# Kernel tuning notes

Measured on AMD Instinct MI355X. Metric: run time of the kernel, lower is better.

## Reference

```python
import jax, jax.numpy as jnp
import numpy as np

B, S, H = 2, 2048, 2048
NH, KVH, HD = 16, 4, 128
R = 16
LORA_SCALE = 32.0 / 16.0  # lora_alpha / lora_r
ATTN_SCALE = HD ** -0.5
NEG = -1e9


def setup_inputs() -> dict:
    key = jax.random.key(0)
    ks = jax.random.split(key, 16)
    q_dim, kv_dim = NH * HD, KVH * HD
    # RoPE tables
    inv_freq = 1.0 / (10000.0 ** (jnp.arange(0, HD, 2, dtype=jnp.float32) / HD))
    ang = jnp.arange(S, dtype=jnp.float32)[:, None] * inv_freq[None, :]  # [S, HD/2]
    emb = jnp.concatenate([ang, ang], axis=-1)  # [S, HD]
    cos = jnp.broadcast_to(jnp.cos(emb)[None], (B, S, HD))
    sin = jnp.broadcast_to(jnp.sin(emb)[None], (B, S, HD))
    # additive causal mask [B,1,S,S]
    causal = jnp.triu(jnp.full((S, S), NEG, dtype=jnp.float32), k=1)
    attention_mask = jnp.broadcast_to(causal[None, None], (B, 1, S, S))
    return {
        'hidden_states': jax.random.normal(ks[0], (B, S, H), jnp.float32),
        'cos': cos,
        'sin': sin,
        'attention_mask': attention_mask,
        'q_w': jax.random.normal(ks[1], (q_dim, H), jnp.float32) * 0.02,
        'k_w': jax.random.normal(ks[2], (kv_dim, H), jnp.float32) * 0.02,
        'v_w': jax.random.normal(ks[3], (kv_dim, H), jnp.float32) * 0.02,
        'q_b': jax.random.normal(ks[4], (q_dim,), jnp.float32) * 0.02,
        'k_b': jax.random.normal(ks[5], (kv_dim,), jnp.float32) * 0.02,
        'v_b': jax.random.normal(ks[6], (kv_dim,), jnp.float32) * 0.02,
        'q_A': jax.random.normal(ks[7], (H, R), jnp.float32) * (1.0 / np.sqrt(H)),
        'q_B': jax.random.normal(ks[8], (R, q_dim), jnp.float32) * 0.02,
        'k_A': jax.random.normal(ks[9], (H, R), jnp.float32) * (1.0 / np.sqrt(H)),
        'k_B': jax.random.normal(ks[10], (R, kv_dim), jnp.float32) * 0.02,
        'v_A': jax.random.normal(ks[11], (H, R), jnp.float32) * (1.0 / np.sqrt(H)),
        'v_B': jax.random.normal(ks[12], (R, kv_dim), jnp.float32) * 0.02,
        'o_w': jax.random.normal(ks[13], (H, H), jnp.float32) * 0.02,
    }


def _rotate_half(x):
    x1, x2 = x[..., : HD // 2], x[..., HD // 2:]
    return jnp.concatenate([-x2, x1], axis=-1)


def reference(hidden_states, cos, sin, attention_mask,
              q_w, k_w, v_w, q_b, k_b, v_b,
              q_A, q_B, k_A, k_B, v_A, v_B, o_w):
    x = hidden_states  # dropout p=0 (eval)
    # fused base + LoRA projections
    q = x @ q_w.T + q_b + LORA_SCALE * ((x @ q_A) @ q_B)  # [B,S,NH*HD]
    k = x @ k_w.T + k_b + LORA_SCALE * ((x @ k_A) @ k_B)  # [B,S,KVH*HD]
    v = x @ v_w.T + v_b + LORA_SCALE * ((x @ v_A) @ v_B)
    q = q.reshape(B, S, NH, HD).transpose(0, 2, 1, 3)   # [B,NH,S,HD]
    k = k.reshape(B, S, KVH, HD).transpose(0, 2, 1, 3)  # [B,KVH,S,HD]
    v = v.reshape(B, S, KVH, HD).transpose(0, 2, 1, 3)
    # RoPE
    c = cos[:, None]  # [B,1,S,HD]
    s = sin[:, None]
    q = q * c + _rotate_half(q) * s
    k = k * c + _rotate_half(k) * s
    # GQA: repeat kv heads
    n_rep = NH // KVH
    k = jnp.repeat(k, n_rep, axis=1)  # [B,NH,S,HD]
    v = jnp.repeat(v, n_rep, axis=1)
    scores = jnp.einsum('bhqd,bhkd->bhqk', q, k) * ATTN_SCALE
    scores = scores + attention_mask
    attn = jax.nn.softmax(scores.astype(jnp.float32), axis=-1).astype(q.dtype)
    out = jnp.einsum('bhqk,bhkd->bhqd', attn, v)
    out = out.transpose(0, 2, 1, 3).reshape(B, S, NH * HD)  # [B,S,H]
    return out @ o_w.T
```

## Files before the change

kernel.cpp:

```cpp
#include <hip/hip_runtime.h>

constexpr int cB   = 2;
constexpr int cS   = 2048;
constexpr int cH   = 2048;
constexpr int cNH  = 16;
constexpr int cKVH = 4;
constexpr int cHD  = 128;
constexpr int cQD  = 2048;
constexpr int cKVD = 512;
constexpr int cNQKV = 3072;
constexpr int cNTOK = 4096;
#define ATTN_SCALE 0.08838834764831845f

typedef __bf16 bf16;
typedef __attribute__((ext_vector_type(8))) __bf16 bf16x8;
typedef __attribute__((ext_vector_type(4))) __bf16 bf16x4;
typedef __attribute__((ext_vector_type(4))) float  f32x4;

__device__ __forceinline__ void async_load16(const bf16* g, bf16* l) {
    __builtin_amdgcn_global_load_lds(
        (const __attribute__((address_space(1))) void*)g,
        (__attribute__((address_space(3))) void*)l, 16, 0, 0);
}

__global__ void conv_f32_bf16(const float* __restrict__ in, bf16* __restrict__ out) {
    int i = (blockIdx.x * 256 + threadIdx.x) * 4;
    f32x4 v = *(const f32x4*)(in + i);
    bf16x4 o;
    o[0] = (bf16)v[0]; o[1] = (bf16)v[1]; o[2] = (bf16)v[2]; o[3] = (bf16)v[3];
    *(bf16x4*)(out + i) = o;
}

__global__ void prep_w(const float* __restrict__ qw, const float* __restrict__ kw, const float* __restrict__ vw,
                       const float* __restrict__ qA, const float* __restrict__ qB,
                       const float* __restrict__ kA, const float* __restrict__ kB,
                       const float* __restrict__ vA, const float* __restrict__ vB,
                       bf16* __restrict__ Wc) {
    const int idx = blockIdx.x * 256 + threadIdx.x;
    const int n = idx >> 11, k = idx & 2047;
    const float* W; const float* Am; const float* Bm; int nn, nd;
    if (n < cQD)             { W = qw; Am = qA; Bm = qB; nn = n;          nd = cQD; }
    else if (n < cQD + cKVD) { W = kw; Am = kA; Bm = kB; nn = n - cQD;    nd = cKVD; }
    else                     { W = vw; Am = vA; Bm = vB; nn = n - cQD - cKVD; nd = cKVD; }
    float acc = 0.f;
    #pragma unroll
    for (int r = 0; r < 16; ++r) acc += Am[k * 16 + r] * Bm[r * nd + nn];
    Wc[(size_t)n * cH + k] = (bf16)(W[(size_t)nn * cH + k] + 2.0f * acc);
}

__global__ void prep_bias(const float* __restrict__ qb, const float* __restrict__ kb,
                          const float* __restrict__ vb, float* __restrict__ biasc) {
    int n = blockIdx.x * 256 + threadIdx.x;
    if (n >= cNQKV) return;
    biasc[n] = (n < cQD) ? qb[n] : (n < cQD + cKVD ? kb[n - cQD] : vb[n - cQD - cKVD]);
}

__global__ __launch_bounds__(256) void gemm_qkv(const bf16* __restrict__ A, const bf16* __restrict__ Bw,
                                                const float* __restrict__ bias,
                                                const float* __restrict__ cosb, const float* __restrict__ sinb,
                                                bf16* __restrict__ Qr, bf16* __restrict__ Kr,
                                                bf16* __restrict__ Vt) {
    __shared__ bf16 Al[128 * 32];
    __shared__ bf16 Bl[128 * 32];
    const int tid = threadIdx.x;
    const int wave = tid >> 6, lane = tid & 63;
    const int quad = lane >> 4, l16 = lane & 15;
    const int wr = wave >> 1, wc = wave & 1;
    const long bm = (long)blockIdx.y * 128, bn = (long)blockIdx.x * 128;
    const int K = cH;

    f32x4 acc[4][4];
    #pragma unroll
    for (int i = 0; i < 4; ++i)
        #pragma unroll
        for (int c = 0; c < 4; ++c) acc[i][c] = f32x4{0.f, 0.f, 0.f, 0.f};

    const int r0 = lane >> 2;
    const int kc = (lane & 3) * 8;

    for (int k0 = 0; k0 < K; k0 += 32) {
        __syncthreads();
        #pragma unroll
        for (int j = 0; j < 2; ++j) {
            const int rb = (wave * 2 + j) * 16;
            const int row = rb + r0;
            async_load16(A  + (size_t)(bm + row) * K + k0 + kc, &Al[rb * 32 + r0 * 32 + kc]);
            async_load16(Bw + (size_t)(bn + row) * K + k0 + kc, &Bl[rb * 32 + r0 * 32 + kc]);
        }
        __syncthreads();
        bf16x8 af[4], bfr[4];
        #pragma unroll
        for (int i = 0; i < 4; ++i) af[i]  = *(const bf16x8*)&Al[(wr * 64 + i * 16 + l16) * 32 + quad * 8];
        #pragma unroll
        for (int c = 0; c < 4; ++c) {
            const int nrow = wc * 32 + (c & 1) * 16 + (c >> 1) * 64 + l16;
            bfr[c] = *(const bf16x8*)&Bl[nrow * 32 + quad * 8];
        }
        #pragma unroll
        for (int i = 0; i < 4; ++i)
            #pragma unroll
            for (int c = 0; c < 4; ++c)
                acc[i][c] = __builtin_amdgcn_mfma_f32_16x16x32_bf16(af[i], bfr[c], acc[i][c], 0, 0, 0);
    }

    #pragma unroll
    for (int c = 0; c < 4; ++c) {
        const int nloc = wc * 32 + (c & 1) * 16 + (c >> 1) * 64 + l16;
        const float bv = bias[bn + nloc];
        #pragma unroll
        for (int i = 0; i < 4; ++i)
            #pragma unroll
            for (int r = 0; r < 4; ++r) acc[i][c][r] += bv;
    }

    const int head = (int)(bn >> 7);
    if (head < cNH + cKVH) {
        const bool isQ = head < cNH;
        #pragma unroll
        for (int cl = 0; cl < 2; ++cl) {
            const int d = wc * 32 + cl * 16 + l16;
            #pragma unroll
            for (int i = 0; i < 4; ++i)
                #pragma unroll
                for (int r = 0; r < 4; ++r) {
                    const long t = bm + wr * 64 + i * 16 + quad * 4 + r;
                    const float cv = cosb[t * cHD + d];
                    const float sv = sinb[t * cHD + d];
                    const float v1 = acc[i][cl][r], v2 = acc[i][cl + 2][r];
                    float o1 = v1 * cv - v2 * sv;
                    float o2 = v2 * cv + v1 * sv;
                    if (isQ) { o1 *= ATTN_SCALE; o2 *= ATTN_SCALE; }
                    const int b = (int)(t >> 11), s = (int)(t & 2047);
                    bf16* dst = isQ
                        ? Qr + ((size_t)(b * cNH + head) * cS + s) * cHD
                        : Kr + ((size_t)(b * cKVH + (head - cNH)) * cS + s) * cHD;
                    dst[d]      = (bf16)o1;
                    dst[d + 64] = (bf16)o2;
                }
        }
    } else {
        const int kv = head - cNH - cKVH;
        const int b = (int)(bm >> 11);
        const int sbase = (int)(bm & 2047);
        #pragma unroll
        for (int c = 0; c < 4; ++c) {
            const int d = wc * 32 + (c & 1) * 16 + (c >> 1) * 64 + l16;
            #pragma unroll
            for (int i = 0; i < 4; ++i) {
                const int s0 = sbase + wr * 64 + i * 16 + quad * 4;
                bf16x4 o4;
                #pragma unroll
                for (int r = 0; r < 4; ++r) o4[r] = (bf16)acc[i][c][r];
                *(bf16x4*)&Vt[((size_t)((b * cKVH + kv) * cHD) + d) * cS + s0] = o4;
            }
        }
    }
}

__global__ __launch_bounds__(256) void gemm_bt_f32(const bf16* __restrict__ A, const bf16* __restrict__ Bw,
                                                   float* __restrict__ Cp, int M, int N, int K) {
    __shared__ bf16 Al[128 * 32];
    __shared__ bf16 Bl[128 * 32];
    const int tid = threadIdx.x;
    const int wave = tid >> 6, lane = tid & 63;
    const int quad = lane >> 4, l16 = lane & 15;
    const int wr = wave >> 1, wc = wave & 1;
    const long bm = (long)blockIdx.y * 128, bn = (long)blockIdx.x * 128;

    f32x4 acc[4][4];
    #pragma unroll
    for (int i = 0; i < 4; ++i)
        #pragma unroll
        for (int c = 0; c < 4; ++c) acc[i][c] = f32x4{0.f, 0.f, 0.f, 0.f};

    const int r0 = lane >> 2;
    const int kc = (lane & 3) * 8;

    for (int k0 = 0; k0 < K; k0 += 32) {
        __syncthreads();
        #pragma unroll
        for (int j = 0; j < 2; ++j) {
            const int rb = (wave * 2 + j) * 16;
            const int row = rb + r0;
            async_load16(A  + (size_t)(bm + row) * K + k0 + kc, &Al[rb * 32 + r0 * 32 + kc]);
            async_load16(Bw + (size_t)(bn + row) * K + k0 + kc, &Bl[rb * 32 + r0 * 32 + kc]);
        }
        __syncthreads();
        bf16x8 af[4], bfr[4];
        #pragma unroll
        for (int i = 0; i < 4; ++i) af[i]  = *(const bf16x8*)&Al[(wr * 64 + i * 16 + l16) * 32 + quad * 8];
        #pragma unroll
        for (int c = 0; c < 4; ++c) bfr[c] = *(const bf16x8*)&Bl[(wc * 64 + c * 16 + l16) * 32 + quad * 8];
        #pragma unroll
        for (int i = 0; i < 4; ++i)
            #pragma unroll
            for (int c = 0; c < 4; ++c)
                acc[i][c] = __builtin_amdgcn_mfma_f32_16x16x32_bf16(af[i], bfr[c], acc[i][c], 0, 0, 0);
    }

    #pragma unroll
    for (int i = 0; i < 4; ++i)
        #pragma unroll
        for (int c = 0; c < 4; ++c) {
            const long m0 = bm + wr * 64 + i * 16 + quad * 4;
            const long n  = bn + wc * 64 + c * 16 + l16;
            #pragma unroll
            for (int r = 0; r < 4; ++r)
                Cp[(m0 + r) * N + n] = acc[i][c][r];
        }
}

__global__ __launch_bounds__(256, 2) void flash4(const bf16* __restrict__ Q, const bf16* __restrict__ K,
                                                 const bf16* __restrict__ Vt, bf16* __restrict__ Ob) {
    __shared__ bf16 kb[8192];
    __shared__ bf16 vb[8192];
    __shared__ bf16 pb[4096];
    const int tid = threadIdx.x;
    const int wave = tid >> 6, lane = tid & 63;
    const int quad = lane >> 4, l16 = lane & 15;
    const int pi = blockIdx.x;
    const int h = blockIdx.y, b = blockIdx.z;

    const bf16* Qh = Q  + (size_t)(b * cNH + h) * cS * cHD;
    const bf16* Kg = K  + (size_t)(b * cKVH + (h >> 2)) * cS * cHD;
    const bf16* Vg = Vt + (size_t)(b * cKVH + (h >> 2)) * cHD * cS;

    int kgo[4], vgo[4], slo[4];
    #pragma unroll
    for (int i2 = 0; i2 < 4; ++i2) {
        const int si = i2 * 256 + tid;
        const int krow = si >> 4, kcsw = si & 15;
        const int kc = (kcsw & 8) | ((kcsw & 7) ^ (krow & 7));
        kgo[i2] = krow * cHD + kc * 8;
        const int vrow = si >> 3, vcsw = si & 7;
        const int vc = vcsw ^ (vrow & 7);
        vgo[i2] = vrow * cS + vc * 8;
        slo[i2] = si * 8;
    }

    #pragma unroll
    for (int t2 = 0; t2 < 2; ++t2) {
        const int qt = t2 == 0 ? (31 - pi) : pi;

        const bf16* Qg = Qh + (size_t)qt * 64 * cHD;
        bf16x8 qf[4];
        #pragma unroll
        for (int ks = 0; ks < 4; ++ks)
            qf[ks] = *(const bf16x8*)(Qg + (size_t)(wave * 16 + l16) * cHD + ks * 32 + quad * 8);

        f32x4 oac[8];
        #pragma unroll
        for (int dt = 0; dt < 8; ++dt) oac[dt] = f32x4{0.f, 0.f, 0.f, 0.f};
        float m_ = -3.0e38f, l_ = 0.f;

        const int nkt = qt + 1;
        for (int kt = 0; kt < nkt; ++kt) {
            __syncthreads();
            const bf16* Kt  = Kg + (size_t)kt * 64 * cHD;
            const bf16* Vtt = Vg + kt * 64;
            #pragma unroll
            for (int i2 = 0; i2 < 4; ++i2) async_load16(Kt + kgo[i2], kb + slo[i2]);
            #pragma unroll
            for (int i2 = 0; i2 < 4; ++i2) async_load16(Vtt + vgo[i2], vb + slo[i2]);
            __syncthreads();

            f32x4 st[4];
            #pragma unroll
            for (int mt = 0; mt < 4; ++mt) {
                bf16x8 kf[4];
                #pragma unroll
                for (int ks = 0; ks < 4; ++ks) {
                    const int c = ks * 4 + quad;
                    const int csw = (c & 8) | ((c & 7) ^ (l16 & 7));
                    kf[ks] = *(const bf16x8*)&kb[(mt * 16 + l16) * 128 + csw * 8];
                }
                f32x4 a = f32x4{0.f, 0.f, 0.f, 0.f};
                #pragma unroll
                for (int ks = 0; ks < 4; ++ks)
                    a = __builtin_amdgcn_mfma_f32_16x16x32_bf16(kf[ks], qf[ks], a, 0, 0, 0);
                st[mt] = a;
            }

            const int qpos = qt * 64 + wave * 16 + l16;
            const bool dm = (kt * 64 + 63) > (qt * 64 + wave * 16);
            float tmax = -3.0e38f;
            #pragma unroll
            for (int mt = 0; mt < 4; ++mt)
                #pragma unroll
                for (int r = 0; r < 4; ++r) {
                    float v = st[mt][r];
                    if (dm) {
                        const int kpos = kt * 64 + mt * 16 + quad * 4 + r;
                        if (kpos > qpos) v = -3.0e38f;
                    }
                    st[mt][r] = v;
                    tmax = fmaxf(tmax, v);
                }
            tmax = fmaxf(tmax, __shfl_xor(tmax, 16, 64));
            tmax = fmaxf(tmax, __shfl_xor(tmax, 32, 64));
            const float mnew = fmaxf(m_, tmax);
            const float alpha = __expf(m_ - mnew);
            m_ = mnew;
            float rs = 0.f;
            #pragma unroll
            for (int mt = 0; mt < 4; ++mt)
                #pragma unroll
                for (int r = 0; r < 4; ++r) {
                    const float p = __expf(st[mt][r] - mnew);
                    st[mt][r] = p;
                    rs += p;
                }
            rs += __shfl_xor(rs, 16, 64);
            rs += __shfl_xor(rs, 32, 64);
            l_ = l_ * alpha + rs;
            #pragma unroll
            for (int dt = 0; dt < 8; ++dt)
                #pragma unroll
                for (int r = 0; r < 4; ++r) oac[dt][r] *= alpha;

            #pragma unroll
            for (int mt = 0; mt < 4; ++mt) {
                bf16x4 p4;
                #pragma unroll
                for (int r = 0; r < 4; ++r) p4[r] = (bf16)st[mt][r];
                const int csw = (mt * 2 + (quad >> 1)) ^ (l16 & 7);
                *(bf16x4*)&pb[wave * 1024 + l16 * 64 + csw * 8 + (quad & 1) * 4] = p4;
            }

            bf16x8 pf[2];
            #pragma unroll
            for (int ks = 0; ks < 2; ++ks) {
                const int c = ks * 4 + quad;
                const int csw = c ^ (l16 & 7);
                pf[ks] = *(const bf16x8*)&pb[wave * 1024 + l16 * 64 + csw * 8];
            }
            #pragma unroll
            for (int dt = 0; dt < 8; ++dt) {
                bf16x8 vf[2];
                #pragma unroll
                for (int ks = 0; ks < 2; ++ks) {
                    const int c = ks * 4 + quad;
                    const int csw = c ^ (l16 & 7);
                    vf[ks] = *(const bf16x8*)&vb[(dt * 16 + l16) * 64 + csw * 8];
                }
                #pragma unroll
                for (int ks = 0; ks < 2; ++ks)
                    oac[dt] = __builtin_amdgcn_mfma_f32_16x16x32_bf16(vf[ks], pf[ks], oac[dt], 0, 0, 0);
            }
        }

        const float inv = 1.0f / l_;
        const int token = qt * 64 + wave * 16 + l16;
        bf16* orow = Ob + (size_t)(b * cS + token) * (cNH * cHD) + h * cHD;
        #pragma unroll
        for (int dt = 0; dt < 8; ++dt) {
            bf16x4 o4;
            #pragma unroll
            for (int r = 0; r < 4; ++r) o4[r] = (bf16)(oac[dt][r] * inv);
            *(bf16x4*)&orow[dt * 16 + quad * 4] = o4;
        }
    }
}

extern "C" void kernel_launch(void* const* d_in, const int* in_sizes, int n_in,
                              void* d_out, int out_size, void* d_ws, size_t ws_size,
                              hipStream_t stream) {
    const float* x    = (const float*)d_in[0];
    const float* cosb = (const float*)d_in[1];
    const float* sinb = (const float*)d_in[2];
    const float* qw = (const float*)d_in[4];
    const float* kw = (const float*)d_in[5];
    const float* vw = (const float*)d_in[6];
    const float* qb = (const float*)d_in[7];
    const float* kb_ = (const float*)d_in[8];
    const float* vb = (const float*)d_in[9];
    const float* qA = (const float*)d_in[10];
    const float* qB = (const float*)d_in[11];
    const float* kA = (const float*)d_in[12];
    const float* kB = (const float*)d_in[13];
    const float* vA = (const float*)d_in[14];
    const float* vB = (const float*)d_in[15];
    const float* ow = (const float*)d_in[16];
    float* out = (float*)d_out;

    char* ws = (char*)d_ws;
    bf16* Xbf   = (bf16*)ws;  ws += (size_t)cNTOK * cH * 2;
    bf16* Wc    = (bf16*)ws;  ws += (size_t)cNQKV * cH * 2;
    float* biasc = (float*)ws; ws += (size_t)cNQKV * 4;
    bf16* Qr    = (bf16*)ws;  ws += (size_t)cB * cNH * cS * cHD * 2;
    bf16* Kr    = (bf16*)ws;  ws += (size_t)cB * cKVH * cS * cHD * 2;
    bf16* Vt    = (bf16*)ws;  ws += (size_t)cB * cKVH * cHD * cS * 2;
    bf16* OWbf  = (bf16*)ws;  ws += (size_t)cH * cH * 2;
    bf16* Aout  = (bf16*)ws;  ws += (size_t)cNTOK * cQD * 2;

    conv_f32_bf16<<<(cNTOK * cH) / 1024, 256, 0, stream>>>(x, Xbf);
    conv_f32_bf16<<<(cH * cH) / 1024, 256, 0, stream>>>(ow, OWbf);
    prep_w<<<(cNQKV * cH) / 256, 256, 0, stream>>>(qw, kw, vw, qA, qB, kA, kB, vA, vB, Wc);
    prep_bias<<<(cNQKV + 255) / 256, 256, 0, stream>>>(qb, kb_, vb, biasc);

    gemm_qkv<<<dim3(cNQKV / 128, cNTOK / 128), 256, 0, stream>>>(Xbf, Wc, biasc, cosb, sinb, Qr, Kr, Vt);

    flash4<<<dim3(16, cNH, cB), 256, 0, stream>>>(Qr, Kr, Vt, Aout);

    gemm_bt_f32<<<dim3(cH / 128, cNTOK / 128), 256, 0, stream>>>(Aout, OWbf, out, cNTOK, cH, cH);
}
```

Before: 406.8 us.

## Share K/V tiles across two GQA heads in flash kernel and vectorize weight prep

The flash attention kernel now handles two query heads of the same KV group per block, so each K/V tile loaded into LDS feeds twice the MMA work. The grid changes from paired q-tiles per block to one q-tile per block. Softmax switches to exp2 with log2(e) folded into the Q scale, and the accumulator rescale is skipped when no row max changes. The LoRA weight merge and bias kernels are fused into one kernel with vectorized loads. The cost is more registers and LDS per block, which could reduce occupancy.

```diff
diff --git a/kernel.cpp b/kernel.cpp
--- a/kernel.cpp
+++ b/kernel.cpp
@@ -11,6 +11,7 @@
 constexpr int cNQKV = 3072;
 constexpr int cNTOK = 4096;
 #define ATTN_SCALE 0.08838834764831845f
+#define QSCALE 0.12751589549581288f
 
 typedef __bf16 bf16;
 typedef __attribute__((ext_vector_type(8))) __bf16 bf16x8;
@@ -31,28 +32,40 @@
     *(bf16x4*)(out + i) = o;
 }
 
-__global__ void prep_w(const float* __restrict__ qw, const float* __restrict__ kw, const float* __restrict__ vw,
-                       const float* __restrict__ qA, const float* __restrict__ qB,
-                       const float* __restrict__ kA, const float* __restrict__ kB,
-                       const float* __restrict__ vA, const float* __restrict__ vB,
-                       bf16* __restrict__ Wc) {
-    const int idx = blockIdx.x * 256 + threadIdx.x;
-    const int n = idx >> 11, k = idx & 2047;
-    const float* W; const float* Am; const float* Bm; int nn, nd;
-    if (n < cQD)             { W = qw; Am = qA; Bm = qB; nn = n;          nd = cQD; }
-    else if (n < cQD + cKVD) { W = kw; Am = kA; Bm = kB; nn = n - cQD;    nd = cKVD; }
-    else                     { W = vw; Am = vA; Bm = vB; nn = n - cQD - cKVD; nd = cKVD; }
-    float acc = 0.f;
-    #pragma unroll
-    for (int r = 0; r < 16; ++r) acc += Am[k * 16 + r] * Bm[r * nd + nn];
-    Wc[(size_t)n * cH + k] = (bf16)(W[(size_t)nn * cH + k] + 2.0f * acc);
-}
-
-__global__ void prep_bias(const float* __restrict__ qb, const float* __restrict__ kb,
-                          const float* __restrict__ vb, float* __restrict__ biasc) {
-    int n = blockIdx.x * 256 + threadIdx.x;
-    if (n >= cNQKV) return;
-    biasc[n] = (n < cQD) ? qb[n] : (n < cQD + cKVD ? kb[n - cQD] : vb[n - cQD - cKVD]);
+__global__ __launch_bounds__(256) void prep_w2(
+        const float* __restrict__ qw, const float* __restrict__ kw, const float* __restrict__ vw,
+        const float* __restrict__ qA, const float* __restrict__ qB,
+        const float* __restrict__ kA, const float* __restrict__ kB,
+        const float* __restrict__ vA, const float* __restrict__ vB,
+        const float* __restrict__ qb, const float* __restrict__ kbias, const float* __restrict__ vb,
+        bf16* __restrict__ Wc, float* __restrict__ biasc) {
+    const int wave = threadIdx.x >> 6, lane = threadIdx.x & 63;
+    const int n = blockIdx.y * 4 + wave;
+    const int k0 = blockIdx.x * 512 + lane * 8;
+    const float* W; const float* Am; const float* Bm; const float* bias; int nn, nd;
+    if (n < cQD)             { W = qw; Am = qA; Bm = qB; bias = qb;    nn = n;               nd = cQD; }
+    else if (n < cQD + cKVD) { W = kw; Am = kA; Bm = kB; bias = kbias; nn = n - cQD;         nd = cKVD; }
+    else                     { W = vw; Am = vA; Bm = vB; bias = vb;    nn = n - cQD - cKVD;  nd = cKVD; }
+    if (blockIdx.x == 0 && lane == 0) biasc[n] = bias[nn];
+    float bm[16];
+    #pragma unroll
+    for (int r = 0; r < 16; ++r) bm[r] = Bm[r * nd + nn];
+    const float* wrow = W + (size_t)nn * cH + k0;
+    f32x4 w0 = *(const f32x4*)(wrow);
+    f32x4 w1 = *(const f32x4*)(wrow + 4);
+    bf16x8 o;
+    #pragma unroll
+    for (int j = 0; j < 8; ++j) {
+        const f32x4* am = (const f32x4*)(Am + (size_t)(k0 + j) * 16);
+        f32x4 a0 = am[0], a1 = am[1], a2 = am[2], a3 = am[3];
+        float acc = 0.f;
+        #pragma unroll
+        for (int c = 0; c < 4; ++c) acc += a0[c] * bm[c] + a1[c] * bm[4 + c]
+                                         + a2[c] * bm[8 + c] + a3[c] * bm[12 + c];
+        const float wv = (j < 4) ? w0[j] : w1[j - 4];
+        o[j] = (bf16)(wv + 2.0f * acc);
+    }
+    *(bf16x8*)&Wc[(size_t)n * cH + k0] = o;
 }
 
 __global__ __launch_bounds__(256) void gemm_qkv(const bf16* __restrict__ A, const bf16* __restrict__ Bw,
@@ -129,7 +142,7 @@
                     const float v1 = acc[i][cl][r], v2 = acc[i][cl + 2][r];
                     float o1 = v1 * cv - v2 * sv;
                     float o2 = v2 * cv + v1 * sv;
-                    if (isQ) { o1 *= ATTN_SCALE; o2 *= ATTN_SCALE; }
+                    if (isQ) { o1 *= QSCALE; o2 *= QSCALE; }
                     const int b = (int)(t >> 11), s = (int)(t & 2047);
                     bf16* dst = isQ
                         ? Qr + ((size_t)(b * cNH + head) * cS + s) * cHD
@@ -210,20 +223,34 @@
         }
 }
 
-__global__ __launch_bounds__(256, 2) void flash4(const bf16* __restrict__ Q, const bf16* __restrict__ K,
+__global__ __launch_bounds__(256, 2) void flash5(const bf16* __restrict__ Q, const bf16* __restrict__ K,
                                                  const bf16* __restrict__ Vt, bf16* __restrict__ Ob) {
     __shared__ bf16 kb[8192];
     __shared__ bf16 vb[8192];
-    __shared__ bf16 pb[4096];
+    __shared__ bf16 pb[8192];
     const int tid = threadIdx.x;
     const int wave = tid >> 6, lane = tid & 63;
     const int quad = lane >> 4, l16 = lane & 15;
-    const int pi = blockIdx.x;
-    const int h = blockIdx.y, b = blockIdx.z;
-
-    const bf16* Qh = Q  + (size_t)(b * cNH + h) * cS * cHD;
-    const bf16* Kg = K  + (size_t)(b * cKVH + (h >> 2)) * cS * cHD;
-    const bf16* Vg = Vt + (size_t)(b * cKVH + (h >> 2)) * cHD * cS;
+    const int l = blockIdx.x;
+    const int xx = l & 15;
+    const int hp = (l >> 4) & 7;
+    const int b  = (l >> 7) & 1;
+    const int half = l >> 8;
+    const int qt = half ? xx : (31 - xx);
+    const int hg = hp >> 1;
+    const int h0 = hg * 4 + (hp & 1) * 2;
+
+    const bf16* Qg0 = Q + ((size_t)(b * cNH + h0)     * cS + qt * 64) * cHD;
+    const bf16* Qg1 = Q + ((size_t)(b * cNH + h0 + 1) * cS + qt * 64) * cHD;
+    const bf16* Kg  = K  + (size_t)(b * cKVH + hg) * cS * cHD;
+    const bf16* Vg  = Vt + (size_t)(b * cKVH + hg) * cHD * cS;
+
+    bf16x8 qf[2][4];
+    #pragma unroll
+    for (int ks = 0; ks < 4; ++ks) {
+        qf[0][ks] = *(const bf16x8*)(Qg0 + (size_t)(wave * 16 + l16) * cHD + ks * 32 + quad * 8);
+        qf[1][ks] = *(const bf16x8*)(Qg1 + (size_t)(wave * 16 + l16) * cHD + ks * 32 + quad * 8);
+    }
 
     int kgo[4], vgo[4], slo[4];
     #pragma unroll
@@ -238,125 +265,132 @@
         slo[i2] = si * 8;
     }
 
-    #pragma unroll
-    for (int t2 = 0; t2 < 2; ++t2) {
-        const int qt = t2 == 0 ? (31 - pi) : pi;
-
-        const bf16* Qg = Qh + (size_t)qt * 64 * cHD;
-        bf16x8 qf[4];
-        #pragma unroll
-        for (int ks = 0; ks < 4; ++ks)
-            qf[ks] = *(const bf16x8*)(Qg + (size_t)(wave * 16 + l16) * cHD + ks * 32 + quad * 8);
-
-        f32x4 oac[8];
-        #pragma unroll
-        for (int dt = 0; dt < 8; ++dt) oac[dt] = f32x4{0.f, 0.f, 0.f, 0.f};
-        float m_ = -3.0e38f, l_ = 0.f;
-
-        const int nkt = qt + 1;
-        for (int kt = 0; kt < nkt; ++kt) {
-            __syncthreads();
-            const bf16* Kt  = Kg + (size_t)kt * 64 * cHD;
-            const bf16* Vtt = Vg + kt * 64;
-            #pragma unroll
-            for (int i2 = 0; i2 < 4; ++i2) async_load16(Kt + kgo[i2], kb + slo[i2]);
-            #pragma unroll
-            for (int i2 = 0; i2 < 4; ++i2) async_load16(Vtt + vgo[i2], vb + slo[i2]);
-            __syncthreads();
-
-            f32x4 st[4];
-            #pragma unroll
-            for (int mt = 0; mt < 4; ++mt) {
-                bf16x8 kf[4];
-                #pragma unroll
-                for (int ks = 0; ks < 4; ++ks) {
-                    const int c = ks * 4 + quad;
-                    const int csw = (c & 8) | ((c & 7) ^ (l16 & 7));
-                    kf[ks] = *(const bf16x8*)&kb[(mt * 16 + l16) * 128 + csw * 8];
+    f32x4 oac[2][8];
+    #pragma unroll
+    for (int e = 0; e < 2; ++e)
+        #pragma unroll
+        for (int dt = 0; dt < 8; ++dt) oac[e][dt] = f32x4{0.f, 0.f, 0.f, 0.f};
+    float m_[2] = {-3.0e38f, -3.0e38f}, l_[2] = {0.f, 0.f};
+
+    const int nkt = qt + 1;
+    for (int kt = 0; kt < nkt; ++kt) {
+        __syncthreads();
+        const bf16* Kt  = Kg + (size_t)kt * 64 * cHD;
+        const bf16* Vtt = Vg + kt * 64;
+        #pragma unroll
+        for (int i2 = 0; i2 < 4; ++i2) async_load16(Kt + kgo[i2], kb + slo[i2]);
+        #pragma unroll
+        for (int i2 = 0; i2 < 4; ++i2) async_load16(Vtt + vgo[i2], vb + slo[i2]);
+        __syncthreads();
+
+        f32x4 st[2][4];
+        #pragma unroll
+        for (int mt = 0; mt < 4; ++mt) {
+            bf16x8 kf[4];
+            #pragma unroll
+            for (int ks = 0; ks < 4; ++ks) {
+                const int c = ks * 4 + quad;
+                const int csw = (c & 8) | ((c & 7) ^ (l16 & 7));
+                kf[ks] = *(const bf16x8*)&kb[(mt * 16 + l16) * 128 + csw * 8];
+            }
+            f32x4 a0 = f32x4{0.f, 0.f, 0.f, 0.f};
+            f32x4 a1 = f32x4{0.f, 0.f, 0.f, 0.f};
+            #pragma unroll
+            for (int ks = 0; ks < 4; ++ks) {
+                a0 = __builtin_amdgcn_mfma_f32_16x16x32_bf16(kf[ks], qf[0][ks], a0, 0, 0, 0);
+                a1 = __builtin_amdgcn_mfma_f32_16x16x32_bf16(kf[ks], qf[1][ks], a1, 0, 0, 0);
+            }
+            st[0][mt] = a0; st[1][mt] = a1;
+        }
+
+        const int qpos = qt * 64 + wave * 16 + l16;
+        if ((kt * 64 + 63) > (qt * 64 + wave * 16)) {
+            #pragma unroll
+            for (int mt = 0; mt < 4; ++mt)
+                #pragma unroll
+                for (int r = 0; r < 4; ++r) {
+                    const int kpos = kt * 64 + mt * 16 + quad * 4 + r;
+                    if (kpos > qpos) { st[0][mt][r] = -3.0e38f; st[1][mt][r] = -3.0e38f; }
                 }
-                f32x4 a = f32x4{0.f, 0.f, 0.f, 0.f};
-                #pragma unroll
-                for (int ks = 0; ks < 4; ++ks)
-                    a = __builtin_amdgcn_mfma_f32_16x16x32_bf16(kf[ks], qf[ks], a, 0, 0, 0);
-                st[mt] = a;
-            }
-
-            const int qpos = qt * 64 + wave * 16 + l16;
-            const bool dm = (kt * 64 + 63) > (qt * 64 + wave * 16);
+        }
+
+        #pragma unroll
+        for (int e = 0; e < 2; ++e) {
             float tmax = -3.0e38f;
             #pragma unroll
             for (int mt = 0; mt < 4; ++mt)
                 #pragma unroll
-                for (int r = 0; r < 4; ++r) {
-                    float v = st[mt][r];
-                    if (dm) {
-                        const int kpos = kt * 64 + mt * 16 + quad * 4 + r;
-                        if (kpos > qpos) v = -3.0e38f;
-                    }
-                    st[mt][r] = v;
-                    tmax = fmaxf(tmax, v);
-                }
+                for (int r = 0; r < 4; ++r) tmax = fmaxf(tmax, st[e][mt][r]);
             tmax = fmaxf(tmax, __shfl_xor(tmax, 16, 64));
             tmax = fmaxf(tmax, __shfl_xor(tmax, 32, 64));
-            const float mnew = fmaxf(m_, tmax);
-            const float alpha = __expf(m_ - mnew);
-            m_ = mnew;
+            const float mnew = fmaxf(m_[e], tmax);
+            if (__any(tmax > m_[e])) {
+                const float alpha = __builtin_amdgcn_exp2f(m_[e] - mnew);
+                l_[e] *= alpha;
+                #pragma unroll
+                for (int dt = 0; dt < 8; ++dt)
+                    #pragma unroll
+                    for (int r = 0; r < 4; ++r) oac[e][dt][r] *= alpha;
+            }
+            m_[e] = mnew;
             float rs = 0.f;
             #pragma unroll
             for (int mt = 0; mt < 4; ++mt)
                 #pragma unroll
                 for (int r = 0; r < 4; ++r) {
-                    const float p = __expf(st[mt][r] - mnew);
-                    st[mt][r] = p;
+                    const float p = __builtin_amdgcn_exp2f(st[e][mt][r] - mnew);
+                    st[e][mt][r] = p;
                     rs += p;
                 }
             rs += __shfl_xor(rs, 16, 64);
             rs += __shfl_xor(rs, 32, 64);
-            l_ = l_ * alpha + rs;
-            #pragma unroll
-            for (int dt = 0; dt < 8; ++dt)
-                #pragma unroll
-                for (int r = 0; r < 4; ++r) oac[dt][r] *= alpha;
-
+            l_[e] += rs;
             #pragma unroll
             for (int mt = 0; mt < 4; ++mt) {
                 bf16x4 p4;
                 #pragma unroll
-                for (int r = 0; r < 4; ++r) p4[r] = (bf16)st[mt][r];
+                for (int r = 0; r < 4; ++r) p4[r] = (bf16)st[e][mt][r];
                 const int csw = (mt * 2 + (quad >> 1)) ^ (l16 & 7);
-                *(bf16x4*)&pb[wave * 1024 + l16 * 64 + csw * 8 + (quad & 1) * 4] = p4;
-            }
-
-            bf16x8 pf[2];
+                *(bf16x4*)&pb[e * 4096 + wave * 1024 + l16 * 64 + csw * 8 + (quad & 1) * 4] = p4;
+            }
+        }
+
+        bf16x8 pf[2][2];
+        #pragma unroll
+        for (int e = 0; e < 2; ++e)
             #pragma unroll
             for (int ks = 0; ks < 2; ++ks) {
                 const int c = ks * 4 + quad;
                 const int csw = c ^ (l16 & 7);
-                pf[ks] = *(const bf16x8*)&pb[wave * 1024 + l16 * 64 + csw * 8];
-            }
-            #pragma unroll
-            for (int dt = 0; dt < 8; ++dt) {
-                bf16x8 vf[2];
-                #pragma unroll
-                for (int ks = 0; ks < 2; ++ks) {
-                    const int c = ks * 4 + quad;
-                    const int csw = c ^ (l16 & 7);
-                    vf[ks] = *(const bf16x8*)&vb[(dt * 16 + l16) * 64 + csw * 8];
-                }
-                #pragma unroll
-                for (int ks = 0; ks < 2; ++ks)
-                    oac[dt] = __builtin_amdgcn_mfma_f32_16x16x32_bf16(vf[ks], pf[ks], oac[dt], 0, 0, 0);
-            }
-        }
-
-        const float inv = 1.0f / l_;
-        const int token = qt * 64 + wave * 16 + l16;
-        bf16* orow = Ob + (size_t)(b * cS + token) * (cNH * cHD) + h * cHD;
+                pf[e][ks] = *(const bf16x8*)&pb[e * 4096 + wave * 1024 + l16 * 64 + csw * 8];
+            }
+        #pragma unroll
+        for (int dt = 0; dt < 8; ++dt) {
+            bf16x8 vf[2];
+            #pragma unroll
+            for (int ks = 0; ks < 2; ++ks) {
+                const int c = ks * 4 + quad;
+                const int csw = c ^ (l16 & 7);
+                vf[ks] = *(const bf16x8*)&vb[(dt * 16 + l16) * 64 + csw * 8];
+            }
+            #pragma unroll
+            for (int ks = 0; ks < 2; ++ks) {
+                oac[0][dt] = __builtin_amdgcn_mfma_f32_16x16x32_bf16(vf[ks], pf[0][ks], oac[0][dt], 0, 0, 0);
+                oac[1][dt] = __builtin_amdgcn_mfma_f32_16x16x32_bf16(vf[ks], pf[1][ks], oac[1][dt], 0, 0, 0);
+            }
+        }
+    }
+
+    const int token = qt * 64 + wave * 16 + l16;
+    #pragma unroll
+    for (int e = 0; e < 2; ++e) {
+        const float inv = 1.0f / l_[e];
+        bf16* orow = Ob + (size_t)(b * cS + token) * (cNH * cHD) + (h0 + e) * cHD;
         #pragma unroll
         for (int dt = 0; dt < 8; ++dt) {
             bf16x4 o4;
             #pragma unroll
-            for (int r = 0; r < 4; ++r) o4[r] = (bf16)(oac[dt][r] * inv);
+            for (int r = 0; r < 4; ++r) o4[r] = (bf16)(oac[e][dt][r] * inv);
             *(bf16x4*)&orow[dt * 16 + quad * 4] = o4;
         }
     }
@@ -395,12 +429,12 @@
 
     conv_f32_bf16<<<(cNTOK * cH) / 1024, 256, 0, stream>>>(x, Xbf);
     conv_f32_bf16<<<(cH * cH) / 1024, 256, 0, stream>>>(ow, OWbf);
-    prep_w<<<(cNQKV * cH) / 256, 256, 0, stream>>>(qw, kw, vw, qA, qB, kA, kB, vA, vB, Wc);
-    prep_bias<<<(cNQKV + 255) / 256, 256, 0, stream>>>(qb, kb_, vb, biasc);
+    prep_w2<<<dim3(cH / 512, cNQKV / 4), 256, 0, stream>>>(qw, kw, vw, qA, qB, kA, kB, vA, vB,
+                                                           qb, kb_, vb, Wc, biasc);
 
     gemm_qkv<<<dim3(cNQKV / 128, cNTOK / 128), 256, 0, stream>>>(Xbf, Wc, biasc, cosb, sinb, Qr, Kr, Vt);
 
-    flash4<<<dim3(16, cNH, cB), 256, 0, stream>>>(Qr, Kr, Vt, Aout);
+    flash5<<<dim3(512), 256, 0, stream>>>(Qr, Kr, Vt, Aout);
 
     gemm_bt_f32<<<dim3(cH / 128, cNTOK / 128), 256, 0, stream>>>(Aout, OWbf, out, cNTOK, cH, cH);
 }
```

After: 422.4 us. 1.04x slower.
